# Kernel tuning notes

Measured on AMD Instinct MI355X. Metric: run time of the kernel, lower is better.

Reference implementation:

```python
import math
import jax, jax.numpy as jnp
import numpy as np

NUM_EXPERTS = 8
ROUTER_TEMP = 1.5
CAP_FACTOR_EVAL = 1.5  # eval mode (self.training == False, no noise)
EPS = 1e-12


def setup_inputs() -> dict:
    key = jax.random.key(0)
    k1, k2 = jax.random.split(key)
    N, C, H, W = 8192, 32, 8, 8
    X = jax.random.normal(k1, (N, C, H, W), dtype=jnp.float32)
    logits = jax.random.normal(k2, (N, NUM_EXPERTS), dtype=jnp.float32)
    return {"X": X, "logits": logits}


def _route(logits_raw, N):
    """Specialized top-1 routing (eval mode). logits_raw: [N, E] raw gate output."""
    E = NUM_EXPERTS
    # clamp + temperature (as in forward before _specialized_routing)
    logits = jnp.clip(logits_raw, -10.0, 10.0) / ROUTER_TEMP

    # z loss: mean(square(logsumexp))
    z_loss = jnp.mean(jnp.square(jax.nn.logsumexp(logits, axis=-1)))

    # diversity loss: L2-normalize columns (dim=0), E x E correlation, off-diag sq
    col_norm = jnp.clip(jnp.linalg.norm(logits, axis=0, keepdims=True), EPS)
    ln = logits / col_norm
    corr = ln.T @ ln  # [E, E]
    off = corr * (1.0 - jnp.eye(E, dtype=logits.dtype))
    div_loss = jnp.sum(off ** 2) / (E * (E - 1))

    probs = jax.nn.softmax(logits, axis=1)  # [N, E]
    expert_idx = jnp.argmax(probs, axis=1)  # [N]
    expert_prob = jnp.take_along_axis(probs, expert_idx[:, None], axis=1)[:, 0]  # [N]
    expert_mask = jax.nn.one_hot(expert_idx, E, dtype=probs.dtype)  # [N, E]

    # aux (load-balance) loss
    f = expert_mask.mean(axis=0)
    p = probs.mean(axis=0)
    aux_loss = jnp.sum(f * p) * E

    # capacity-constrained position assignment via argsort + cumsum
    Ccap = max(1, math.ceil(CAP_FACTOR_EVAL * N / E))
    order = jnp.argsort(-expert_prob)            # descending by prob
    mask_sorted = expert_mask[order]             # [N, E]
    pos_sorted = jnp.cumsum(mask_sorted, axis=0) - 1.0
    within = (pos_sorted < Ccap).astype(probs.dtype)
    mask_sorted = mask_sorted * within
    unsort = jnp.argsort(order)                  # inverse permutation
    mask = mask_sorted[unsort]                   # [N, E]

    gate = expert_prob * mask.sum(axis=-1)       # [N]
    pos_idx = jnp.clip(pos_sorted, 0.0, Ccap - 1).astype(jnp.int32)[unsort]  # [N, E]
    one_hot_pos = jax.nn.one_hot(pos_idx, Ccap, dtype=probs.dtype)           # [N, E, Ccap]
    combine = gate[:, None, None] * mask[:, :, None] * one_hot_pos           # [N, E, Ccap]
    return combine, z_loss, aux_loss, div_loss


def reference(X, logits):
    N = X.shape[0]
    combine, z_loss, aux_loss, div_loss = _route(logits, N)
    dispatch = combine > 0  # bool [N, E, Ccap]
    logits_std = jnp.std(logits, ddof=1)  # torch .std() is unbiased
    return dispatch, combine, z_loss, aux_loss, div_loss, logits_std
```

## Files before the change

kernel.cpp:

```cpp
#include <hip/hip_runtime.h>
#include <math.h>

#define NN 8192
#define NE 8

typedef float f32x4 __attribute__((ext_vector_type(4)));

#define WS_KEY_OFF  512
#define WS_RANK_OFF (512 + 65536)

#define WREDUCE(q, expr)                              \
    do {                                              \
        double v_ = (expr);                           \
        v_ += __shfl_down(v_, 32);                    \
        v_ += __shfl_down(v_, 16);                    \
        v_ += __shfl_down(v_, 8);                     \
        v_ += __shfl_down(v_, 4);                     \
        v_ += __shfl_down(v_, 2);                     \
        v_ += __shfl_down(v_, 1);                     \
        if (lane == 0) part[q][wv] = v_;              \
    } while (0)

__global__ __launch_bounds__(256) void kzero_kernel(f32x4* __restrict__ out, size_t n4) {
    const size_t i = (size_t)blockIdx.x * 256 + threadIdx.x;
    if (i < n4) {
        const f32x4 z = {0.f, 0.f, 0.f, 0.f};
        out[i] = z;
    }
}

__global__ __launch_bounds__(256) void krow_kernel(const float* __restrict__ logits,
                                                   double* __restrict__ sums,
                                                   unsigned long long* __restrict__ key) {
    __shared__ double part[55][4];
    const int n = blockIdx.x * 256 + threadIdx.x;
    const int lane = threadIdx.x & 63;
    const int wv = threadIdx.x >> 6;

    const float4* lp = reinterpret_cast<const float4*>(logits) + (size_t)n * 2;
    float4 a = lp[0];
    float4 b = lp[1];
    float lr[NE] = {a.x, a.y, a.z, a.w, b.x, b.y, b.z, b.w};

    double raw_s = 0.0, raw_q = 0.0;
#pragma unroll
    for (int e = 0; e < NE; ++e) {
        raw_s += (double)lr[e];
        raw_q += (double)lr[e] * (double)lr[e];
    }

    float l[NE];
#pragma unroll
    for (int e = 0; e < NE; ++e)
        l[e] = fminf(fmaxf(lr[e], -10.0f), 10.0f) / 1.5f;

    float m = l[0];
#pragma unroll
    for (int e = 1; e < NE; ++e) m = fmaxf(m, l[e]);

    double ex[NE], s = 0.0;
#pragma unroll
    for (int e = 0; e < NE; ++e) {
        ex[e] = exp((double)(l[e] - m));
        s += ex[e];
    }
    double p[NE];
    float pf[NE];
#pragma unroll
    for (int e = 0; e < NE; ++e) {
        p[e] = ex[e] / s;
        pf[e] = (float)p[e];
    }

    int idx = 0;
    float best = pf[0];
#pragma unroll
    for (int e = 1; e < NE; ++e)
        if (pf[e] > best) { best = pf[e]; idx = e; }

    double lse = (double)m + log(s);

    unsigned int pb = __float_as_uint(best);
    key[n] = ((unsigned long long)pb << 16) |
             ((unsigned long long)(8191 - n) << 3) | (unsigned int)idx;

    WREDUCE(0, lse * lse);
#pragma unroll
    for (int e = 0; e < NE; ++e) WREDUCE(1 + e, p[e]);
#pragma unroll
    for (int e = 0; e < NE; ++e) WREDUCE(9 + e, (idx == e) ? 1.0 : 0.0);
    WREDUCE(17, raw_s);
    WREDUCE(18, raw_q);
    {
        int q = 19;
#pragma unroll
        for (int e = 0; e < NE; ++e)
#pragma unroll
            for (int f = 0; f < NE; ++f)
                if (f >= e) { WREDUCE(q, (double)l[e] * (double)l[f]); ++q; }
    }
    __syncthreads();
    if (threadIdx.x < 55) {
        double t = part[threadIdx.x][0] + part[threadIdx.x][1] +
                   part[threadIdx.x][2] + part[threadIdx.x][3];
        atomicAdd(&sums[threadIdx.x], t);
    }
}

__global__ void kfin_kernel(const double* __restrict__ sums, float* __restrict__ outs) {
    if (threadIdx.x != 0 || blockIdx.x != 0) return;
    const double Nd = (double)NN;
    double z_loss = sums[0] / Nd;

    double aux = 0.0;
    for (int e = 0; e < NE; ++e)
        aux += (sums[9 + e] / Nd) * (sums[1 + e] / Nd);
    aux *= (double)NE;

    double S[NE][NE];
    int q = 19;
    for (int e = 0; e < NE; ++e)
        for (int f = e; f < NE; ++f) {
            S[e][f] = sums[q];
            S[f][e] = sums[q];
            ++q;
        }
    double nrm[NE];
    for (int e = 0; e < NE; ++e) nrm[e] = fmax(sqrt(S[e][e]), 1e-12);
    double dv = 0.0;
    for (int e = 0; e < NE; ++e)
        for (int f = 0; f < NE; ++f)
            if (e != f) {
                double c = S[e][f] / (nrm[e] * nrm[f]);
                dv += c * c;
            }
    dv /= (double)(NE * (NE - 1));

    const double M = Nd * (double)NE;
    double var = (sums[18] - sums[17] * sums[17] / M) / (M - 1.0);

    outs[0] = (float)z_loss;
    outs[1] = (float)aux;
    outs[2] = (float)dv;
    outs[3] = (float)sqrt(var);
}

__global__ __launch_bounds__(256) void krank_kernel(const unsigned long long* __restrict__ key,
                                                    int* __restrict__ rank) {
    __shared__ unsigned long long kk[256];
    const int tid = threadIdx.x;
    const int n = blockIdx.x * 256 + tid;
    kk[tid] = key[blockIdx.y * 256 + tid];
    __syncthreads();
    const unsigned long long kn = key[n];
    const unsigned int e = (unsigned int)(kn & 7ull);
    int cnt = 0;
#pragma unroll 8
    for (int j = 0; j < 256; ++j) {
        unsigned long long km = kk[j];
        cnt += (int)(((km & 7ull) == e) & (km > kn));
    }
    if (cnt) atomicAdd(&rank[n], cnt);
}

__global__ __launch_bounds__(256) void kscatter_kernel(const unsigned long long* __restrict__ key,
                                                       const int* __restrict__ rank,
                                                       float* __restrict__ out, int Ccap) {
    const int n = blockIdx.x * 256 + threadIdx.x;
    const unsigned long long kn = key[n];
    const int e = (int)(kn & 7ull);
    const float p = __uint_as_float((unsigned int)(kn >> 16));
    const int r = rank[n];
    if (r < Ccap) {
        size_t off = ((size_t)n * NE + e) * (size_t)Ccap + (size_t)r;
        out[off] = 1.0f;
        out[(size_t)NN * NE * Ccap + off] = p;
    }
}

extern "C" void kernel_launch(void* const* d_in, const int* in_sizes, int n_in,
                              void* d_out, int out_size, void* d_ws, size_t ws_size,
                              hipStream_t stream) {
    const float* logits = (const float*)d_in[1];
    float* out = (float*)d_out;

    const int Ccap = (out_size - 4) / (2 * NN * NE);
    const size_t big = (size_t)2 * NN * NE * (size_t)Ccap;

    double* sums = (double*)d_ws;
    unsigned long long* key = (unsigned long long*)((char*)d_ws + WS_KEY_OFF);
    int* rank = (int*)((char*)d_ws + WS_RANK_OFF);

    (void)hipMemsetAsync(d_ws, 0, WS_RANK_OFF + NN * sizeof(int), stream);

    const size_t n4 = (size_t)out_size / 4;
    const int fill_blocks = (int)((n4 + 255) / 256);
    kzero_kernel<<<fill_blocks, 256, 0, stream>>>((f32x4*)out, n4);

    krow_kernel<<<NN / 256, 256, 0, stream>>>(logits, sums, key);
    kfin_kernel<<<1, 64, 0, stream>>>(sums, out + big);
    krank_kernel<<<dim3(NN / 256, NN / 256), 256, 0, stream>>>(key, rank);
    kscatter_kernel<<<NN / 256, 256, 0, stream>>>(key, rank, out, Ccap);
}
```

Measured before the change: 813.1 us.

## Fuse rank, scatter and finalize kernels; replace atomics with per-block partial sums

Merges the rank-counting, scatter and loss-finalization kernels into one kernel. Each of 32 blocks now loops over all key tiles instead of launching a 32x32 grid with atomic rank accumulation. Per-block partial sums replace the global double atomics, and the workspace memset is dropped. This removes launches, the memset and atomics, but parallelism for the O(N^2) rank pass drops from 1024 blocks to 32.

```diff
diff --git a/kernel.cpp b/kernel.cpp
--- a/kernel.cpp
+++ b/kernel.cpp
@@ -3,11 +3,11 @@
 
 #define NN 8192
 #define NE 8
+#define NBLK 32
 
 typedef float f32x4 __attribute__((ext_vector_type(4)));
 
-#define WS_KEY_OFF  512
-#define WS_RANK_OFF (512 + 65536)
+#define WS_PSUM_OFF 65536
 
 #define WREDUCE(q, expr)                              \
     do {                                              \
@@ -30,7 +30,7 @@
 }
 
 __global__ __launch_bounds__(256) void krow_kernel(const float* __restrict__ logits,
-                                                   double* __restrict__ sums,
+                                                   double* __restrict__ psums,
                                                    unsigned long long* __restrict__ key) {
     __shared__ double part[55][4];
     const int n = blockIdx.x * 256 + threadIdx.x;
@@ -100,38 +100,73 @@
                 if (f >= e) { WREDUCE(q, (double)l[e] * (double)l[f]); ++q; }
     }
     __syncthreads();
-    if (threadIdx.x < 55) {
-        double t = part[threadIdx.x][0] + part[threadIdx.x][1] +
-                   part[threadIdx.x][2] + part[threadIdx.x][3];
-        atomicAdd(&sums[threadIdx.x], t);
-    }
-}
-
-__global__ void kfin_kernel(const double* __restrict__ sums, float* __restrict__ outs) {
-    if (threadIdx.x != 0 || blockIdx.x != 0) return;
+    if (threadIdx.x < 55)
+        psums[(size_t)blockIdx.x * 55 + threadIdx.x] =
+            part[threadIdx.x][0] + part[threadIdx.x][1] +
+            part[threadIdx.x][2] + part[threadIdx.x][3];
+}
+
+__global__ __launch_bounds__(256) void kfran_kernel(const unsigned long long* __restrict__ key,
+                                                    const double* __restrict__ psums,
+                                                    float* __restrict__ out, int Ccap) {
+    __shared__ unsigned long long kk[256];
+    __shared__ double sums[55];
+    const int tid = threadIdx.x;
+    const int n = blockIdx.x * 256 + tid;
+    const unsigned long long kn = key[n];
+    const unsigned int e = (unsigned int)(kn & 7ull);
+    int cnt = 0;
+    for (int c = 0; c < NBLK; ++c) {
+        __syncthreads();
+        kk[tid] = key[c * 256 + tid];
+        __syncthreads();
+#pragma unroll 8
+        for (int j = 0; j < 256; ++j) {
+            unsigned long long km = kk[j];
+            cnt += (int)(((km & 7ull) == e) & (km > kn));
+        }
+    }
+    const float p = __uint_as_float((unsigned int)(kn >> 16));
+    if (cnt < Ccap) {
+        size_t off = ((size_t)n * NE + (int)e) * (size_t)Ccap + (size_t)cnt;
+        out[off] = 1.0f;
+        out[(size_t)NN * NE * (size_t)Ccap + off] = p;
+    }
+
+    if (blockIdx.x != 0) return;
+    __syncthreads();
+    if (tid < 55) {
+        double t = 0.0;
+        for (int b = 0; b < NBLK; ++b) t += psums[(size_t)b * 55 + tid];
+        sums[tid] = t;
+    }
+    __syncthreads();
+    if (tid != 0) return;
+
+    float* outs = out + (size_t)2 * NN * NE * (size_t)Ccap;
     const double Nd = (double)NN;
     double z_loss = sums[0] / Nd;
 
     double aux = 0.0;
-    for (int e = 0; e < NE; ++e)
-        aux += (sums[9 + e] / Nd) * (sums[1 + e] / Nd);
+    for (int ee = 0; ee < NE; ++ee)
+        aux += (sums[9 + ee] / Nd) * (sums[1 + ee] / Nd);
     aux *= (double)NE;
 
     double S[NE][NE];
     int q = 19;
-    for (int e = 0; e < NE; ++e)
-        for (int f = e; f < NE; ++f) {
-            S[e][f] = sums[q];
-            S[f][e] = sums[q];
+    for (int ee = 0; ee < NE; ++ee)
+        for (int f = ee; f < NE; ++f) {
+            S[ee][f] = sums[q];
+            S[f][ee] = sums[q];
             ++q;
         }
     double nrm[NE];
-    for (int e = 0; e < NE; ++e) nrm[e] = fmax(sqrt(S[e][e]), 1e-12);
+    for (int ee = 0; ee < NE; ++ee) nrm[ee] = fmax(sqrt(S[ee][ee]), 1e-12);
     double dv = 0.0;
-    for (int e = 0; e < NE; ++e)
+    for (int ee = 0; ee < NE; ++ee)
         for (int f = 0; f < NE; ++f)
-            if (e != f) {
-                double c = S[e][f] / (nrm[e] * nrm[f]);
+            if (ee != f) {
+                double c = S[ee][f] / (nrm[ee] * nrm[f]);
                 dv += c * c;
             }
     dv /= (double)(NE * (NE - 1));
@@ -143,39 +178,6 @@
     outs[1] = (float)aux;
     outs[2] = (float)dv;
     outs[3] = (float)sqrt(var);
-}
-
-__global__ __launch_bounds__(256) void krank_kernel(const unsigned long long* __restrict__ key,
-                                                    int* __restrict__ rank) {
-    __shared__ unsigned long long kk[256];
-    const int tid = threadIdx.x;
-    const int n = blockIdx.x * 256 + tid;
-    kk[tid] = key[blockIdx.y * 256 + tid];
-    __syncthreads();
-    const unsigned long long kn = key[n];
-    const unsigned int e = (unsigned int)(kn & 7ull);
-    int cnt = 0;
-#pragma unroll 8
-    for (int j = 0; j < 256; ++j) {
-        unsigned long long km = kk[j];
-        cnt += (int)(((km & 7ull) == e) & (km > kn));
-    }
-    if (cnt) atomicAdd(&rank[n], cnt);
-}
-
-__global__ __launch_bounds__(256) void kscatter_kernel(const unsigned long long* __restrict__ key,
-                                                       const int* __restrict__ rank,
-                                                       float* __restrict__ out, int Ccap) {
-    const int n = blockIdx.x * 256 + threadIdx.x;
-    const unsigned long long kn = key[n];
-    const int e = (int)(kn & 7ull);
-    const float p = __uint_as_float((unsigned int)(kn >> 16));
-    const int r = rank[n];
-    if (r < Ccap) {
-        size_t off = ((size_t)n * NE + e) * (size_t)Ccap + (size_t)r;
-        out[off] = 1.0f;
-        out[(size_t)NN * NE * Ccap + off] = p;
-    }
 }
 
 extern "C" void kernel_launch(void* const* d_in, const int* in_sizes, int n_in,
@@ -185,20 +187,14 @@
     float* out = (float*)d_out;
 
     const int Ccap = (out_size - 4) / (2 * NN * NE);
-    const size_t big = (size_t)2 * NN * NE * (size_t)Ccap;
-
-    double* sums = (double*)d_ws;
-    unsigned long long* key = (unsigned long long*)((char*)d_ws + WS_KEY_OFF);
-    int* rank = (int*)((char*)d_ws + WS_RANK_OFF);
-
-    (void)hipMemsetAsync(d_ws, 0, WS_RANK_OFF + NN * sizeof(int), stream);
+
+    unsigned long long* key = (unsigned long long*)d_ws;
+    double* psums = (double*)((char*)d_ws + WS_PSUM_OFF);
 
     const size_t n4 = (size_t)out_size / 4;
     const int fill_blocks = (int)((n4 + 255) / 256);
     kzero_kernel<<<fill_blocks, 256, 0, stream>>>((f32x4*)out, n4);
 
-    krow_kernel<<<NN / 256, 256, 0, stream>>>(logits, sums, key);
-    kfin_kernel<<<1, 64, 0, stream>>>(sums, out + big);
-    krank_kernel<<<dim3(NN / 256, NN / 256), 256, 0, stream>>>(key, rank);
-    kscatter_kernel<<<NN / 256, 256, 0, stream>>>(key, rank, out, Ccap);
-}
+    krow_kernel<<<NBLK, 256, 0, stream>>>(logits, psums, key);
+    kfran_kernel<<<NBLK, 256, 0, stream>>>(key, psums, out, Ccap);
+}
```

New measurement: 968.3 us. 1.19x slower.
